# Kernel optimization log

Measured on AMD Instinct MI355X. Metric: run time of the kernel, lower is better.

Reference implementation:

```python
import jax, jax.numpy as jnp
import numpy as np

D = 1024
SCALE = 10.0  # forward does qk.div(1/10) == qk * 10


def setup_inputs() -> dict:
    key = jax.random.key(0)
    ks = jax.random.split(key, 9)
    B, S = 8, 2048
    lim = 1.0 / np.sqrt(D)  # torch Linear default init range
    return {
        "query": jax.random.normal(ks[0], (B, S, D), jnp.float32),
        "key": jax.random.normal(ks[1], (B, S, D), jnp.float32),
        "value": jax.random.normal(ks[2], (B, S, D), jnp.float32),
        "Wq": jax.random.uniform(ks[3], (D, D), jnp.float32, -lim, lim),
        "bq": jax.random.uniform(ks[4], (D,), jnp.float32, -lim, lim),
        "Wk": jax.random.uniform(ks[5], (D, D), jnp.float32, -lim, lim),
        "bk": jax.random.uniform(ks[6], (D,), jnp.float32, -lim, lim),
        "Wv": jax.random.uniform(ks[7], (D, D), jnp.float32, -lim, lim),
        "bv": jax.random.uniform(ks[8], (D,), jnp.float32, -lim, lim),
    }


def reference(query, key, value, Wq, bq, Wk, bk, Wv, bv):
    # torch Linear: x @ W.T + b
    q = jnp.einsum("bsd,ed->bse", query, Wq) + bq
    k = jnp.einsum("bsd,ed->bse", key, Wk) + bk
    v = jnp.einsum("bsd,ed->bse", value, Wv) + bv
    qk = jnp.einsum("bqd,bkd->bqk", q, k)
    scaled_qk = qk * SCALE  # qk.div(1.0 / scale_factor)
    softmax_qk = jax.nn.softmax(scaled_qk, axis=-1)
    # dropout in eval mode == identity (deterministic reference)
    output = jnp.einsum("bqk,bkd->bqd", softmax_qk, v)
    return (output, softmax_qk)
```

## Files before the change

### kernel.cpp

```cpp
#include <hip/hip_runtime.h>

typedef unsigned short u16;
typedef unsigned int u32;
typedef __bf16 bf16x8 __attribute__((ext_vector_type(8)));
typedef float f32x4 __attribute__((ext_vector_type(4)));

__device__ __forceinline__ u16 bf16_rne(float f) {
  u32 u = __float_as_uint(f);
  u += 0x7fffu + ((u >> 16) & 1u);
  return (u16)(u >> 16);
}
__device__ __forceinline__ float bf16_to_f(u16 h) {
  return __uint_as_float(((u32)h) << 16);
}
__device__ __forceinline__ void gload16(const u16* g, u16* l) {
  __builtin_amdgcn_global_load_lds(
      (const __attribute__((address_space(1))) void*)g,
      (__attribute__((address_space(3))) void*)l, 16, 0, 0);
}

__global__ __launch_bounds__(256) void split_kernel(const float* __restrict__ x,
                                                    u16* __restrict__ hi,
                                                    u16* __restrict__ lo, int n8) {
  int i = blockIdx.x * 256 + threadIdx.x;
  if (i >= n8) return;
  float4 a = ((const float4*)x)[2 * i];
  float4 b = ((const float4*)x)[2 * i + 1];
  float v[8] = {a.x, a.y, a.z, a.w, b.x, b.y, b.z, b.w};
  union { u16 u[8]; uint4 q; } H, L;
#pragma unroll
  for (int j = 0; j < 8; ++j) H.u[j] = bf16_rne(v[j]);
  ((uint4*)hi)[i] = H.q;
  if (lo != nullptr) {
#pragma unroll
    for (int j = 0; j < 8; ++j) L.u[j] = bf16_rne(v[j] - bf16_to_f(H.u[j]));
    ((uint4*)lo)[i] = L.q;
  }
}

__global__ __launch_bounds__(256) void transpose_split(const float* __restrict__ in,
                                                       u16* __restrict__ hiT,
                                                       u16* __restrict__ loT) {
  __shared__ float tile[32][33];
  const int t = threadIdx.x;
  const int r0 = blockIdx.y * 32, c0 = blockIdx.x * 32;
  const int x = t & 31, y = t >> 5;
#pragma unroll
  for (int i = 0; i < 4; ++i)
    tile[y + i * 8][x] = in[(size_t)(r0 + y + i * 8) * 1024 + c0 + x];
  __syncthreads();
#pragma unroll
  for (int i = 0; i < 4; ++i) {
    float v = tile[x][y + i * 8];
    u16 h = bf16_rne(v);
    u16 l = bf16_rne(v - bf16_to_f(h));
    size_t o = (size_t)(c0 + y + i * 8) * 1024 + r0 + x;
    hiT[o] = h;
    loT[o] = l;
  }
}

__global__ __launch_bounds__(256) void zero_vec(float* __restrict__ h) {
  h[blockIdx.x * 256 + threadIdx.x] = 0.f;
}

__global__ __launch_bounds__(256) void colvec_kernel(const float* __restrict__ W,
                                                     const float* __restrict__ b,
                                                     float* __restrict__ h) {
  __shared__ float sb[16];
  const int t = threadIdx.x;
  const int e0 = blockIdx.x * 16;
  if (t < 16) sb[t] = b[e0 + t];
  __syncthreads();
  float a0 = 0.f, a1 = 0.f, a2 = 0.f, a3 = 0.f;
#pragma unroll
  for (int i = 0; i < 16; ++i) {
    const float* row = W + (size_t)(e0 + i) * 1024;
    const float be = sb[i];
    a0 += row[t] * be;
    a1 += row[t + 256] * be;
    a2 += row[t + 512] * be;
    a3 += row[t + 768] * be;
  }
  atomicAdd(&h[t], a0);
  atomicAdd(&h[t + 256], a1);
  atomicAdd(&h[t + 512], a2);
  atomicAdd(&h[t + 768], a3);
}

__global__ __launch_bounds__(256) void rowdot_kernel(const float* __restrict__ X,
                                                     const float* __restrict__ h,
                                                     float* __restrict__ w) {
  const int t = threadIdx.x, lane = t & 63, wv = t >> 6;
  const size_t row = (size_t)blockIdx.x * 4 + wv;
  const float4* xr = (const float4*)(X + row * 1024);
  const float4* hr = (const float4*)h;
  float acc = 0.f;
#pragma unroll
  for (int j = 0; j < 4; ++j) {
    float4 a = xr[lane + j * 64];
    float4 b = hr[lane + j * 64];
    acc += a.x * b.x + a.y * b.y + a.z * b.z + a.w * b.w;
  }
#pragma unroll
  for (int o = 32; o > 0; o >>= 1) acc += __shfl_xor(acc, o, 64);
  if (lane == 0) w[row] = acc;
}

template <int NPROD, int EPI>
__global__ __launch_bounds__(256) void gemm_bt(
    const u16* __restrict__ Ah, const u16* __restrict__ Al,
    const u16* __restrict__ Bh, const u16* __restrict__ Bl,
    const float* __restrict__ bias,
    u16* __restrict__ Ch, u16* __restrict__ Cl,
    float* __restrict__ Cf, float scale, int K,
    int lda, int ldb, int ldc,
    long long batchA, long long batchB, long long batchC) {
  __shared__ u16 sAh[4096];
  __shared__ u16 sBh[4096];
  __shared__ u16 sAl[NPROD == 3 ? 4096 : 64];
  __shared__ u16 sBl[NPROD == 3 ? 4096 : 64];

  const int t = threadIdx.x;
  const int w = t >> 6;
  const int lane = t & 63;
  const int m0 = blockIdx.y * 128;
  const int n0 = blockIdx.x * 128;
  const long long z = blockIdx.z;

  Ah += z * batchA;
  Bh += z * batchB;

  const int rS = t >> 2;
  const int cS = (((t & 3) ^ ((t >> 3) & 3))) * 8;
  const u16* pAh = Ah + (size_t)(m0 + rS) * lda + cS;
  const u16* pBh = Bh + (size_t)(n0 + rS) * ldb + cS;
  const u16* pAl = nullptr;
  const u16* pBl = nullptr;
  if constexpr (NPROD == 3) {
    pAl = Al + z * batchA + (size_t)(m0 + rS) * lda + cS;
    pBl = Bl + z * batchB + (size_t)(n0 + rS) * ldb + cS;
  }

  const int wr = (w >> 1) * 64;
  const int wc = (w & 1) * 64;
  const int fr = lane & 15;
  const int cc = lane >> 4;
  const int fk = (cc ^ ((fr >> 1) & 3)) * 8;

  f32x4 acc[4][4];
#pragma unroll
  for (int i = 0; i < 4; ++i)
#pragma unroll
    for (int j = 0; j < 4; ++j) acc[i][j] = (f32x4){0.f, 0.f, 0.f, 0.f};

  for (int k0 = 0; k0 < K; k0 += 32) {
    __syncthreads();
#pragma unroll
    for (int j = 0; j < 2; ++j) {
      gload16(pAh + (size_t)j * 64 * lda + k0, &sAh[j * 2048 + w * 512]);
      gload16(pBh + (size_t)j * 64 * ldb + k0, &sBh[j * 2048 + w * 512]);
      if constexpr (NPROD == 3) {
        gload16(pAl + (size_t)j * 64 * lda + k0, &sAl[j * 2048 + w * 512]);
        gload16(pBl + (size_t)j * 64 * ldb + k0, &sBl[j * 2048 + w * 512]);
      }
    }
    __syncthreads();
    bf16x8 ah[4], bh[4], al[4], bl[4];
#pragma unroll
    for (int i = 0; i < 4; ++i) {
      ah[i] = *(const bf16x8*)&sAh[(wr + i * 16 + fr) * 32 + fk];
      bh[i] = *(const bf16x8*)&sBh[(wc + i * 16 + fr) * 32 + fk];
      if constexpr (NPROD == 3) {
        al[i] = *(const bf16x8*)&sAl[(wr + i * 16 + fr) * 32 + fk];
        bl[i] = *(const bf16x8*)&sBl[(wc + i * 16 + fr) * 32 + fk];
      }
    }
#pragma unroll
    for (int i = 0; i < 4; ++i)
#pragma unroll
      for (int j = 0; j < 4; ++j) {
        acc[i][j] = __builtin_amdgcn_mfma_f32_16x16x32_bf16(ah[i], bh[j], acc[i][j], 0, 0, 0);
        if constexpr (NPROD == 3) {
          acc[i][j] = __builtin_amdgcn_mfma_f32_16x16x32_bf16(ah[i], bl[j], acc[i][j], 0, 0, 0);
          acc[i][j] = __builtin_amdgcn_mfma_f32_16x16x32_bf16(al[i], bh[j], acc[i][j], 0, 0, 0);
        }
      }
  }

  if constexpr (EPI >= 2) Cf += z * batchC;

#pragma unroll
  for (int i = 0; i < 4; ++i) {
    const int row0 = m0 + wr + i * 16 + ((lane >> 4) << 2);
#pragma unroll
    for (int j = 0; j < 4; ++j) {
      const int col = n0 + wc + j * 16 + (lane & 15);
      if constexpr (EPI == 0) {
        const float b = bias ? bias[col] : 0.0f;
#pragma unroll
        for (int r = 0; r < 4; ++r) {
          float c = acc[i][j][r] + b;
          u16 h = bf16_rne(c);
          u16 l = bf16_rne(c - bf16_to_f(h));
          size_t o = (size_t)(row0 + r) * ldc + col;
          Ch[o] = h;
          Cl[o] = l;
        }
      } else if constexpr (EPI == 1) {
        const float b = bias[col];
        ushort4 pk;
        pk.x = bf16_rne(acc[i][j][0] + b);
        pk.y = bf16_rne(acc[i][j][1] + b);
        pk.z = bf16_rne(acc[i][j][2] + b);
        pk.w = bf16_rne(acc[i][j][3] + b);
        const int bb = row0 >> 11;
        const int s = row0 & 2047;
        *(ushort4*)&Ch[(size_t)bb * 2097152 + (size_t)col * 2048 + s] = pk;
      } else if constexpr (EPI == 2) {
#pragma unroll
        for (int r = 0; r < 4; ++r)
          Cf[(size_t)(row0 + r) * ldc + col] = acc[i][j][r] * scale;
      } else {
        const float wv = bias[(size_t)z * 2048 + col];
#pragma unroll
        for (int r = 0; r < 4; ++r)
          Cf[(size_t)(row0 + r) * ldc + col] = (acc[i][j][r] + wv) * scale;
      }
    }
  }
}

template <int NPROD, int EPI>
__global__ __launch_bounds__(512) void gemm256(
    const u16* __restrict__ Ah, const u16* __restrict__ Al,
    const u16* __restrict__ Bh, const u16* __restrict__ Bl,
    const float* __restrict__ bias,
    u16* __restrict__ Ch, u16* __restrict__ Cl,
    float* __restrict__ Cf, float scale, int K,
    int lda, int ldb, int ldc,
    long long batchA, long long batchB, long long batchC) {
  __shared__ u16 sAh[2][8192];
  __shared__ u16 sBh[2][8192];
  __shared__ u16 sAl[NPROD == 3 ? 16384 : 8];
  __shared__ u16 sBl[NPROD == 3 ? 16384 : 8];

  const int t = threadIdx.x;
  const int w = t >> 6;
  const int lane = t & 63;
  const int m0 = blockIdx.y * 256;
  const int n0 = blockIdx.x * 256;
  const long long z = blockIdx.z;

  const int rS = t >> 2;
  const int cS = ((t & 3) ^ ((rS >> 1) & 3)) * 8;
  const u16* pAh = Ah + z * batchA + (size_t)(m0 + rS) * lda + cS;
  const u16* pBh = Bh + z * batchB + (size_t)(n0 + rS) * ldb + cS;
  const u16* pAl = nullptr;
  const u16* pBl = nullptr;
  if constexpr (NPROD == 3) {
    pAl = Al + z * batchA + (size_t)(m0 + rS) * lda + cS;
    pBl = Bl + z * batchB + (size_t)(n0 + rS) * ldb + cS;
  }

  const int wr = (w >> 2) * 128;
  const int wc = (w & 3) * 64;
  const int fr = lane & 15;
  const int fk = (((lane >> 4) ^ ((fr >> 1) & 3)) * 8);

  f32x4 acc[8][4];
#pragma unroll
  for (int i = 0; i < 8; ++i)
#pragma unroll
    for (int j = 0; j < 4; ++j) acc[i][j] = (f32x4){0.f, 0.f, 0.f, 0.f};

  auto STAGE = [&](int b, int k0) {
    gload16(pAh + k0, &sAh[b][w * 512]);
    gload16(pAh + (size_t)128 * lda + k0, &sAh[b][4096 + w * 512]);
    gload16(pBh + k0, &sBh[b][w * 512]);
    gload16(pBh + (size_t)128 * ldb + k0, &sBh[b][4096 + w * 512]);
    if constexpr (NPROD == 3) {
      gload16(pAl + k0, &sAl[b * 8192 + w * 512]);
      gload16(pAl + (size_t)128 * lda + k0, &sAl[b * 8192 + 4096 + w * 512]);
      gload16(pBl + k0, &sBl[b * 8192 + w * 512]);
      gload16(pBl + (size_t)128 * ldb + k0, &sBl[b * 8192 + 4096 + w * 512]);
    }
  };

  STAGE(0, 0);
  const int nt = K >> 5;
  for (int kt = 0; kt < nt; ++kt) {
    const int cur = kt & 1;
    asm volatile("s_waitcnt lgkmcnt(0)\n\ts_barrier" ::: "memory");
    if (kt + 1 < nt) {
      STAGE(cur ^ 1, (kt + 1) << 5);
      if constexpr (NPROD == 3)
        asm volatile("s_waitcnt vmcnt(8)" ::: "memory");
      else
        asm volatile("s_waitcnt vmcnt(4)" ::: "memory");
    } else {
      asm volatile("s_waitcnt vmcnt(0)" ::: "memory");
    }
    asm volatile("s_barrier" ::: "memory");

    bf16x8 bh[4], bl[4];
#pragma unroll
    for (int n = 0; n < 4; ++n) {
      bh[n] = *(const bf16x8*)&sBh[cur][(wc + n * 16 + fr) * 32 + fk];
      if constexpr (NPROD == 3)
        bl[n] = *(const bf16x8*)&sBl[cur * 8192 + (wc + n * 16 + fr) * 32 + fk];
    }
#pragma unroll
    for (int q = 0; q < 4; ++q) {
      bf16x8 a0h = *(const bf16x8*)&sAh[cur][(wr + (2 * q) * 16 + fr) * 32 + fk];
      bf16x8 a1h = *(const bf16x8*)&sAh[cur][(wr + (2 * q + 1) * 16 + fr) * 32 + fk];
      bf16x8 a0l, a1l;
      if constexpr (NPROD == 3) {
        a0l = *(const bf16x8*)&sAl[cur * 8192 + (wr + (2 * q) * 16 + fr) * 32 + fk];
        a1l = *(const bf16x8*)&sAl[cur * 8192 + (wr + (2 * q + 1) * 16 + fr) * 32 + fk];
      }
      __builtin_amdgcn_s_setprio(1);
#pragma unroll
      for (int n = 0; n < 4; ++n) {
        acc[2 * q][n] = __builtin_amdgcn_mfma_f32_16x16x32_bf16(a0h, bh[n], acc[2 * q][n], 0, 0, 0);
        acc[2 * q + 1][n] = __builtin_amdgcn_mfma_f32_16x16x32_bf16(a1h, bh[n], acc[2 * q + 1][n], 0, 0, 0);
      }
      if constexpr (NPROD == 3) {
#pragma unroll
        for (int n = 0; n < 4; ++n) {
          acc[2 * q][n] = __builtin_amdgcn_mfma_f32_16x16x32_bf16(a0h, bl[n], acc[2 * q][n], 0, 0, 0);
          acc[2 * q + 1][n] = __builtin_amdgcn_mfma_f32_16x16x32_bf16(a1h, bl[n], acc[2 * q + 1][n], 0, 0, 0);
        }
#pragma unroll
        for (int n = 0; n < 4; ++n) {
          acc[2 * q][n] = __builtin_amdgcn_mfma_f32_16x16x32_bf16(a0l, bh[n], acc[2 * q][n], 0, 0, 0);
          acc[2 * q + 1][n] = __builtin_amdgcn_mfma_f32_16x16x32_bf16(a1l, bh[n], acc[2 * q + 1][n], 0, 0, 0);
        }
      }
      __builtin_amdgcn_s_setprio(0);
      if (q < 3) asm volatile("s_barrier");
    }
  }

  if constexpr (EPI >= 2) Cf += z * batchC;

#pragma unroll
  for (int i = 0; i < 8; ++i) {
    const int row0 = m0 + wr + i * 16 + ((lane >> 4) << 2);
#pragma unroll
    for (int j = 0; j < 4; ++j) {
      const int col = n0 + wc + j * 16 + (lane & 15);
      if constexpr (EPI == 0) {
        const float bsv = bias ? bias[col] : 0.0f;
#pragma unroll
        for (int r = 0; r < 4; ++r) {
          float c = acc[i][j][r] + bsv;
          u16 h = bf16_rne(c);
          u16 l = bf16_rne(c - bf16_to_f(h));
          size_t o = (size_t)(row0 + r) * ldc + col;
          Ch[o] = h;
          Cl[o] = l;
        }
      } else if constexpr (EPI == 1) {
        const float bsv = bias[col];
        ushort4 pk;
        pk.x = bf16_rne(acc[i][j][0] + bsv);
        pk.y = bf16_rne(acc[i][j][1] + bsv);
        pk.z = bf16_rne(acc[i][j][2] + bsv);
        pk.w = bf16_rne(acc[i][j][3] + bsv);
        const int bb = row0 >> 11;
        const int s = row0 & 2047;
        *(ushort4*)&Ch[(size_t)bb * 2097152 + (size_t)col * 2048 + s] = pk;
      } else if constexpr (EPI == 2) {
#pragma unroll
        for (int r = 0; r < 4; ++r)
          Cf[(size_t)(row0 + r) * ldc + col] = acc[i][j][r] * scale;
      } else {
        const float wv = bias[(size_t)z * 2048 + col];
#pragma unroll
        for (int r = 0; r < 4; ++r)
          Cf[(size_t)(row0 + r) * ldc + col] = (acc[i][j][r] + wv) * scale;
      }
    }
  }
}

__global__ __launch_bounds__(256) void softmax_kernel(float* __restrict__ L,
                                                      u16* __restrict__ P) {
  const size_t row = blockIdx.x;
  float* r = L + row * 2048;
  u16* p = P + row * 2048;
  const int t = threadIdx.x;
  const int w = t >> 6;
  const int lane = t & 63;

  float4 v0 = ((const float4*)r)[2 * t];
  float4 v1 = ((const float4*)r)[2 * t + 1];
  float e[8] = {v0.x, v0.y, v0.z, v0.w, v1.x, v1.y, v1.z, v1.w};

  float vm = e[0];
#pragma unroll
  for (int j = 1; j < 8; ++j) vm = fmaxf(vm, e[j]);
#pragma unroll
  for (int o = 32; o > 0; o >>= 1) vm = fmaxf(vm, __shfl_xor(vm, o, 64));
  __shared__ float redm[4], reds[4];
  if (lane == 0) redm[w] = vm;
  __syncthreads();
  vm = fmaxf(fmaxf(redm[0], redm[1]), fmaxf(redm[2], redm[3]));

  float s = 0.f;
#pragma unroll
  for (int j = 0; j < 8; ++j) {
    e[j] = __expf(e[j] - vm);
    s += e[j];
  }
#pragma unroll
  for (int o = 32; o > 0; o >>= 1) s += __shfl_xor(s, o, 64);
  if (lane == 0) reds[w] = s;
  __syncthreads();
  s = reds[0] + reds[1] + reds[2] + reds[3];
  const float inv = 1.0f / s;

  float4 o0, o1;
  o0.x = e[0] * inv; o0.y = e[1] * inv; o0.z = e[2] * inv; o0.w = e[3] * inv;
  o1.x = e[4] * inv; o1.y = e[5] * inv; o1.z = e[6] * inv; o1.w = e[7] * inv;
  ((float4*)r)[2 * t] = o0;
  ((float4*)r)[2 * t + 1] = o1;
  union { u16 u[8]; uint4 q; } pk;
  pk.u[0] = bf16_rne(o0.x); pk.u[1] = bf16_rne(o0.y);
  pk.u[2] = bf16_rne(o0.z); pk.u[3] = bf16_rne(o0.w);
  pk.u[4] = bf16_rne(o1.x); pk.u[5] = bf16_rne(o1.y);
  pk.u[6] = bf16_rne(o1.z); pk.u[7] = bf16_rne(o1.w);
  ((uint4*)p)[t] = pk.q;
}

extern "C" void kernel_launch(void* const* d_in, const int* in_sizes, int n_in,
                              void* d_out, int out_size, void* d_ws, size_t ws_size,
                              hipStream_t stream) {
  const float* Xq = (const float*)d_in[0];
  const float* Xk = (const float*)d_in[1];
  const float* Xv = (const float*)d_in[2];
  const float* Wq = (const float*)d_in[3];
  const float* bq = (const float*)d_in[4];
  const float* Wk = (const float*)d_in[5];
  const float* bk = (const float*)d_in[6];
  const float* Wv = (const float*)d_in[7];
  const float* bv = (const float*)d_in[8];
  (void)bk;

  char* out = (char*)d_out;
  char* ws = (char*)d_ws;

  u16* T_hi = (u16*)(out + 0);
  u16* T_lo = (u16*)(out + 33554432);
  u16* Xq_hi = (u16*)(out + 67108864);
  u16* Xq_lo = (u16*)(out + 100663296);
  u16* Xv_hi = (u16*)(out + 134217728);
  u16* Mt_hi = (u16*)(out + 167772160);
  u16* Mt_lo = (u16*)(out + 171966464);
  float* logits = (float*)(out + 67108864);
  float* outO = (float*)(out + 0);

  u16* WqT_hi = (u16*)(ws + 0);
  u16* WqT_lo = (u16*)(ws + 2097152);
  u16* WkT_hi = (u16*)(ws + 4194304);
  u16* WkT_lo = (u16*)(ws + 6291456);
  u16* Wv_hi = (u16*)(ws + 8388608);
  u16* P = (u16*)(ws + 0);
  float* hvec = (float*)(ws + 67108864);
  float* wvec = (float*)(ws + 67112960);
  u16* Xk_hi = (u16*)(ws + 67178496);
  u16* Xk_lo = (u16*)(ws + 100732928);
  u16* Vt = (u16*)(ws + 134287360);

  transpose_split<<<dim3(32, 32), 256, 0, stream>>>(Wq, WqT_hi, WqT_lo);
  transpose_split<<<dim3(32, 32), 256, 0, stream>>>(Wk, WkT_hi, WkT_lo);
  zero_vec<<<4, 256, 0, stream>>>(hvec);
  colvec_kernel<<<64, 256, 0, stream>>>(Wk, bq, hvec);
  split_kernel<<<512, 256, 0, stream>>>(Wv, Wv_hi, nullptr, 131072);

  split_kernel<<<8192, 256, 0, stream>>>(Xk, Xk_hi, Xk_lo, 2097152);
  rowdot_kernel<<<4096, 256, 0, stream>>>(Xk, hvec, wvec);
  split_kernel<<<8192, 256, 0, stream>>>(Xq, Xq_hi, Xq_lo, 2097152);
  split_kernel<<<8192, 256, 0, stream>>>(Xv, Xv_hi, nullptr, 2097152);

  gemm_bt<3, 0><<<dim3(8, 8, 1), 256, 0, stream>>>(
      WkT_hi, WkT_lo, WqT_hi, WqT_lo, nullptr, Mt_hi, Mt_lo, nullptr, 1.f,
      1024, 1024, 1024, 1024, 0, 0, 0);
  gemm256<1, 1><<<dim3(4, 64, 1), 512, 0, stream>>>(
      Xv_hi, nullptr, Wv_hi, nullptr, bv, Vt, nullptr, nullptr, 1.f,
      1024, 1024, 1024, 1024, 0, 0, 0);
  gemm256<3, 0><<<dim3(4, 64, 1), 512, 0, stream>>>(
      Xq_hi, Xq_lo, Mt_hi, Mt_lo, nullptr, T_hi, T_lo, nullptr, 1.f,
      1024, 1024, 1024, 1024, 0, 0, 0);
  gemm256<3, 3><<<dim3(8, 8, 8), 512, 0, stream>>>(
      T_hi, T_lo, Xk_hi, Xk_lo, wvec, nullptr, nullptr, logits, 10.f,
      1024, 1024, 1024, 2048, 2048LL * 1024, 2048LL * 1024, 2048LL * 2048);
  softmax_kernel<<<16384, 256, 0, stream>>>(logits, P);
  gemm256<1, 2><<<dim3(4, 8, 8), 512, 0, stream>>>(
      P, nullptr, Vt, nullptr, nullptr, nullptr, nullptr, outO, 1.f,
      2048, 2048, 2048, 1024, 2048LL * 2048, 1024LL * 2048, 2048LL * 1024);
}
```

Before: 970.7 us.

## Interleave next-tile global-to-LDS prefetch with MFMA phases in GEMM main loop

Restructures the double-buffered GEMM K-loop so the next tile's global-to-LDS loads are issued in pieces inside the compute phases (hi parts in the first phase, lo parts in the second) rather than all at once at the top of the iteration. Each phase now loads its LDS fragments, issues its prefetch, syncs with a barrier, then runs MFMAs, using sched_barrier to stop the compiler from reordering. The vmcnt wait moves to the end of the iteration. The single-product path is regrouped into two phases of four A fragments each. The goal is to overlap memory latency with MFMA work and spread out load issue, at the cost of more barriers per iteration.

```diff
diff --git a/kernel.cpp b/kernel.cpp
--- a/kernel.cpp
+++ b/kernel.cpp
@@ -274,58 +274,68 @@
 #pragma unroll
     for (int j = 0; j < 4; ++j) acc[i][j] = (f32x4){0.f, 0.f, 0.f, 0.f};
 
-  auto STAGE = [&](int b, int k0) {
+  auto SAH = [&](int b, int k0) {
     gload16(pAh + k0, &sAh[b][w * 512]);
     gload16(pAh + (size_t)128 * lda + k0, &sAh[b][4096 + w * 512]);
+  };
+  auto SBH = [&](int b, int k0) {
     gload16(pBh + k0, &sBh[b][w * 512]);
     gload16(pBh + (size_t)128 * ldb + k0, &sBh[b][4096 + w * 512]);
-    if constexpr (NPROD == 3) {
-      gload16(pAl + k0, &sAl[b * 8192 + w * 512]);
-      gload16(pAl + (size_t)128 * lda + k0, &sAl[b * 8192 + 4096 + w * 512]);
-      gload16(pBl + k0, &sBl[b * 8192 + w * 512]);
-      gload16(pBl + (size_t)128 * ldb + k0, &sBl[b * 8192 + 4096 + w * 512]);
-    }
   };
-
-  STAGE(0, 0);
+  auto SAL = [&](int b, int k0) {
+    gload16(pAl + k0, &sAl[b * 8192 + w * 512]);
+    gload16(pAl + (size_t)128 * lda + k0, &sAl[b * 8192 + 4096 + w * 512]);
+  };
+  auto SBL = [&](int b, int k0) {
+    gload16(pBl + k0, &sBl[b * 8192 + w * 512]);
+    gload16(pBl + (size_t)128 * ldb + k0, &sBl[b * 8192 + 4096 + w * 512]);
+  };
+
+  SAH(0, 0);
+  SBH(0, 0);
+  if constexpr (NPROD == 3) {
+    SAL(0, 0);
+    SBL(0, 0);
+  }
+  asm volatile("s_waitcnt vmcnt(0)" ::: "memory");
+  __builtin_amdgcn_s_barrier();
+
   const int nt = K >> 5;
   for (int kt = 0; kt < nt; ++kt) {
     const int cur = kt & 1;
-    asm volatile("s_waitcnt lgkmcnt(0)\n\ts_barrier" ::: "memory");
-    if (kt + 1 < nt) {
-      STAGE(cur ^ 1, (kt + 1) << 5);
-      if constexpr (NPROD == 3)
-        asm volatile("s_waitcnt vmcnt(8)" ::: "memory");
-      else
-        asm volatile("s_waitcnt vmcnt(4)" ::: "memory");
-    } else {
-      asm volatile("s_waitcnt vmcnt(0)" ::: "memory");
-    }
-    asm volatile("s_barrier" ::: "memory");
-
-    bf16x8 bh[4], bl[4];
-#pragma unroll
-    for (int n = 0; n < 4; ++n) {
-      bh[n] = *(const bf16x8*)&sBh[cur][(wc + n * 16 + fr) * 32 + fk];
-      if constexpr (NPROD == 3)
-        bl[n] = *(const bf16x8*)&sBl[cur * 8192 + (wc + n * 16 + fr) * 32 + fk];
-    }
-#pragma unroll
-    for (int q = 0; q < 4; ++q) {
-      bf16x8 a0h = *(const bf16x8*)&sAh[cur][(wr + (2 * q) * 16 + fr) * 32 + fk];
-      bf16x8 a1h = *(const bf16x8*)&sAh[cur][(wr + (2 * q + 1) * 16 + fr) * 32 + fk];
-      bf16x8 a0l, a1l;
-      if constexpr (NPROD == 3) {
-        a0l = *(const bf16x8*)&sAl[cur * 8192 + (wr + (2 * q) * 16 + fr) * 32 + fk];
-        a1l = *(const bf16x8*)&sAl[cur * 8192 + (wr + (2 * q + 1) * 16 + fr) * 32 + fk];
-      }
-      __builtin_amdgcn_s_setprio(1);
-#pragma unroll
-      for (int n = 0; n < 4; ++n) {
-        acc[2 * q][n] = __builtin_amdgcn_mfma_f32_16x16x32_bf16(a0h, bh[n], acc[2 * q][n], 0, 0, 0);
-        acc[2 * q + 1][n] = __builtin_amdgcn_mfma_f32_16x16x32_bf16(a1h, bh[n], acc[2 * q + 1][n], 0, 0, 0);
-      }
-      if constexpr (NPROD == 3) {
+    const int nxt = cur ^ 1;
+    const bool pf = (kt + 1) < nt;
+    const int kn = (kt + 1) << 5;
+
+    if constexpr (NPROD == 3) {
+      bf16x8 bh[4], bl[4];
+#pragma unroll
+      for (int q = 0; q < 4; ++q) {
+        if (q == 0) {
+#pragma unroll
+          for (int n = 0; n < 4; ++n) {
+            bh[n] = *(const bf16x8*)&sBh[cur][(wc + n * 16 + fr) * 32 + fk];
+            bl[n] = *(const bf16x8*)&sBl[cur * 8192 + (wc + n * 16 + fr) * 32 + fk];
+          }
+        }
+        bf16x8 a0h = *(const bf16x8*)&sAh[cur][(wr + (2 * q) * 16 + fr) * 32 + fk];
+        bf16x8 a1h = *(const bf16x8*)&sAh[cur][(wr + (2 * q + 1) * 16 + fr) * 32 + fk];
+        bf16x8 a0l = *(const bf16x8*)&sAl[cur * 8192 + (wr + (2 * q) * 16 + fr) * 32 + fk];
+        bf16x8 a1l = *(const bf16x8*)&sAl[cur * 8192 + (wr + (2 * q + 1) * 16 + fr) * 32 + fk];
+        if (pf) {
+          if (q == 0) { SAH(nxt, kn); SBH(nxt, kn); }
+          if (q == 1) { SAL(nxt, kn); SBL(nxt, kn); }
+        }
+        __builtin_amdgcn_sched_barrier(0);
+        __builtin_amdgcn_s_barrier();
+        asm volatile("s_waitcnt lgkmcnt(0)" ::: "memory");
+        __builtin_amdgcn_sched_barrier(0);
+        __builtin_amdgcn_s_setprio(1);
+#pragma unroll
+        for (int n = 0; n < 4; ++n) {
+          acc[2 * q][n] = __builtin_amdgcn_mfma_f32_16x16x32_bf16(a0h, bh[n], acc[2 * q][n], 0, 0, 0);
+          acc[2 * q + 1][n] = __builtin_amdgcn_mfma_f32_16x16x32_bf16(a1h, bh[n], acc[2 * q + 1][n], 0, 0, 0);
+        }
 #pragma unroll
         for (int n = 0; n < 4; ++n) {
           acc[2 * q][n] = __builtin_amdgcn_mfma_f32_16x16x32_bf16(a0h, bl[n], acc[2 * q][n], 0, 0, 0);
@@ -336,9 +346,49 @@
           acc[2 * q][n] = __builtin_amdgcn_mfma_f32_16x16x32_bf16(a0l, bh[n], acc[2 * q][n], 0, 0, 0);
           acc[2 * q + 1][n] = __builtin_amdgcn_mfma_f32_16x16x32_bf16(a1l, bh[n], acc[2 * q + 1][n], 0, 0, 0);
         }
-      }
-      __builtin_amdgcn_s_setprio(0);
-      if (q < 3) asm volatile("s_barrier");
+        __builtin_amdgcn_s_setprio(0);
+        __builtin_amdgcn_sched_barrier(0);
+        if (q == 3) {
+          asm volatile("s_waitcnt vmcnt(0)" ::: "memory");
+          __builtin_amdgcn_sched_barrier(0);
+        }
+        __builtin_amdgcn_s_barrier();
+      }
+    } else {
+      bf16x8 bh[4];
+#pragma unroll
+      for (int q = 0; q < 2; ++q) {
+        if (q == 0) {
+#pragma unroll
+          for (int n = 0; n < 4; ++n)
+            bh[n] = *(const bf16x8*)&sBh[cur][(wc + n * 16 + fr) * 32 + fk];
+        }
+        bf16x8 af[4];
+#pragma unroll
+        for (int i = 0; i < 4; ++i)
+          af[i] = *(const bf16x8*)&sAh[cur][(wr + (4 * q + i) * 16 + fr) * 32 + fk];
+        if (pf) {
+          if (q == 0) SAH(nxt, kn);
+          if (q == 1) SBH(nxt, kn);
+        }
+        __builtin_amdgcn_sched_barrier(0);
+        __builtin_amdgcn_s_barrier();
+        asm volatile("s_waitcnt lgkmcnt(0)" ::: "memory");
+        __builtin_amdgcn_sched_barrier(0);
+        __builtin_amdgcn_s_setprio(1);
+#pragma unroll
+        for (int i = 0; i < 4; ++i)
+#pragma unroll
+          for (int n = 0; n < 4; ++n)
+            acc[4 * q + i][n] = __builtin_amdgcn_mfma_f32_16x16x32_bf16(af[i], bh[n], acc[4 * q + i][n], 0, 0, 0);
+        __builtin_amdgcn_s_setprio(0);
+        __builtin_amdgcn_sched_barrier(0);
+        if (q == 1) {
+          asm volatile("s_waitcnt vmcnt(0)" ::: "memory");
+          __builtin_amdgcn_sched_barrier(0);
+        }
+        __builtin_amdgcn_s_barrier();
+      }
     }
   }
 
```

After: 909.4 us. -6.3%, faster.

## Replace 256x256 GEMM tiles with 128x128 tiles and XCD-aware block remap

Applied to the files above, without the earlier changes.

Replaces the 512-thread 256x256-tile GEMM with a 256-thread 128x128-tile version that uses half the LDS per buffer, and restructures the main loop: the prefetch is issued before the wait, with sched_barriers, and a single trailing barrier replaces the per-subtile barriers. It also remaps linear block IDs so consecutive blocks spread across the 8 XCDs in chunks, for better L2 locality. The aim is higher occupancy and more blocks to fill the CUs. The cost is lower arithmetic intensity per tile and more global and L2 traffic.

```diff
diff --git a/kernel.cpp b/kernel.cpp
--- a/kernel.cpp
+++ b/kernel.cpp
@@ -232,7 +232,7 @@
 }
 
 template <int NPROD, int EPI>
-__global__ __launch_bounds__(512) void gemm256(
+__global__ __launch_bounds__(256) void gemm128(
     const u16* __restrict__ Ah, const u16* __restrict__ Al,
     const u16* __restrict__ Bh, const u16* __restrict__ Bl,
     const float* __restrict__ bias,
@@ -240,20 +240,30 @@
     float* __restrict__ Cf, float scale, int K,
     int lda, int ldb, int ldc,
     long long batchA, long long batchB, long long batchC) {
-  __shared__ u16 sAh[2][8192];
-  __shared__ u16 sBh[2][8192];
-  __shared__ u16 sAl[NPROD == 3 ? 16384 : 8];
-  __shared__ u16 sBl[NPROD == 3 ? 16384 : 8];
+  __shared__ u16 sAh[8192];
+  __shared__ u16 sBh[8192];
+  __shared__ u16 sAl[NPROD == 3 ? 8192 : 8];
+  __shared__ u16 sBl[NPROD == 3 ? 8192 : 8];
 
   const int t = threadIdx.x;
   const int w = t >> 6;
   const int lane = t & 63;
-  const int m0 = blockIdx.y * 256;
-  const int n0 = blockIdx.x * 256;
-  const long long z = blockIdx.z;
+
+  const u32 gx = gridDim.x;
+  const u32 gxy = gridDim.x * gridDim.y;
+  const u32 total = gxy * gridDim.z;
+  const u32 h = blockIdx.x + gridDim.x * (blockIdx.y + gridDim.y * blockIdx.z);
+  const u32 l = (h & 7) * (total >> 3) + (h >> 3);
+  const u32 bz = l / gxy;
+  const u32 rem = l - bz * gxy;
+  const u32 by = rem / gx;
+  const u32 bx = rem - by * gx;
+  const int m0 = by * 128;
+  const int n0 = bx * 128;
+  const long long z = bz;
 
   const int rS = t >> 2;
-  const int cS = ((t & 3) ^ ((rS >> 1) & 3)) * 8;
+  const int cS = (((t & 3) ^ ((t >> 3) & 3))) * 8;
   const u16* pAh = Ah + z * batchA + (size_t)(m0 + rS) * lda + cS;
   const u16* pBh = Bh + z * batchB + (size_t)(n0 + rS) * ldb + cS;
   const u16* pAl = nullptr;
@@ -263,37 +273,41 @@
     pBl = Bl + z * batchB + (size_t)(n0 + rS) * ldb + cS;
   }
 
-  const int wr = (w >> 2) * 128;
-  const int wc = (w & 3) * 64;
+  const int wr = (w >> 1) * 64;
+  const int wc = (w & 1) * 64;
   const int fr = lane & 15;
-  const int fk = (((lane >> 4) ^ ((fr >> 1) & 3)) * 8);
-
-  f32x4 acc[8][4];
-#pragma unroll
-  for (int i = 0; i < 8; ++i)
+  const int cc = lane >> 4;
+  const int fk = (cc ^ ((fr >> 1) & 3)) * 8;
+
+  f32x4 acc[4][4];
+#pragma unroll
+  for (int i = 0; i < 4; ++i)
 #pragma unroll
     for (int j = 0; j < 4; ++j) acc[i][j] = (f32x4){0.f, 0.f, 0.f, 0.f};
 
-  auto STAGE = [&](int b, int k0) {
-    gload16(pAh + k0, &sAh[b][w * 512]);
-    gload16(pAh + (size_t)128 * lda + k0, &sAh[b][4096 + w * 512]);
-    gload16(pBh + k0, &sBh[b][w * 512]);
-    gload16(pBh + (size_t)128 * ldb + k0, &sBh[b][4096 + w * 512]);
-    if constexpr (NPROD == 3) {
-      gload16(pAl + k0, &sAl[b * 8192 + w * 512]);
-      gload16(pAl + (size_t)128 * lda + k0, &sAl[b * 8192 + 4096 + w * 512]);
-      gload16(pBl + k0, &sBl[b * 8192 + w * 512]);
-      gload16(pBl + (size_t)128 * ldb + k0, &sBl[b * 8192 + 4096 + w * 512]);
+  auto STAGE = [&](int bo, int k0) {
+#pragma unroll
+    for (int j = 0; j < 2; ++j) {
+      gload16(pAh + (size_t)j * 64 * lda + k0, &sAh[bo + j * 2048 + w * 512]);
+      gload16(pBh + (size_t)j * 64 * ldb + k0, &sBh[bo + j * 2048 + w * 512]);
+      if constexpr (NPROD == 3) {
+        gload16(pAl + (size_t)j * 64 * lda + k0, &sAl[bo + j * 2048 + w * 512]);
+        gload16(pBl + (size_t)j * 64 * ldb + k0, &sBl[bo + j * 2048 + w * 512]);
+      }
     }
   };
 
   STAGE(0, 0);
+
   const int nt = K >> 5;
   for (int kt = 0; kt < nt; ++kt) {
-    const int cur = kt & 1;
-    asm volatile("s_waitcnt lgkmcnt(0)\n\ts_barrier" ::: "memory");
-    if (kt + 1 < nt) {
-      STAGE(cur ^ 1, (kt + 1) << 5);
+    const int bc = (kt & 1) * 4096;
+    const int bn = 4096 - bc;
+    const bool pf = (kt + 1) < nt;
+
+    if (pf) STAGE(bn, (kt + 1) << 5);
+    __builtin_amdgcn_sched_barrier(0);
+    if (pf) {
       if constexpr (NPROD == 3)
         asm volatile("s_waitcnt vmcnt(8)" ::: "memory");
       else
@@ -301,51 +315,40 @@
     } else {
       asm volatile("s_waitcnt vmcnt(0)" ::: "memory");
     }
+    __builtin_amdgcn_sched_barrier(0);
     asm volatile("s_barrier" ::: "memory");
 
-    bf16x8 bh[4], bl[4];
-#pragma unroll
-    for (int n = 0; n < 4; ++n) {
-      bh[n] = *(const bf16x8*)&sBh[cur][(wc + n * 16 + fr) * 32 + fk];
-      if constexpr (NPROD == 3)
-        bl[n] = *(const bf16x8*)&sBl[cur * 8192 + (wc + n * 16 + fr) * 32 + fk];
-    }
-#pragma unroll
-    for (int q = 0; q < 4; ++q) {
-      bf16x8 a0h = *(const bf16x8*)&sAh[cur][(wr + (2 * q) * 16 + fr) * 32 + fk];
-      bf16x8 a1h = *(const bf16x8*)&sAh[cur][(wr + (2 * q + 1) * 16 + fr) * 32 + fk];
-      bf16x8 a0l, a1l;
+    bf16x8 ah[4], bh[4], al[4], bl[4];
+#pragma unroll
+    for (int i = 0; i < 4; ++i) {
+      ah[i] = *(const bf16x8*)&sAh[bc + (wr + i * 16 + fr) * 32 + fk];
+      bh[i] = *(const bf16x8*)&sBh[bc + (wc + i * 16 + fr) * 32 + fk];
       if constexpr (NPROD == 3) {
-        a0l = *(const bf16x8*)&sAl[cur * 8192 + (wr + (2 * q) * 16 + fr) * 32 + fk];
-        a1l = *(const bf16x8*)&sAl[cur * 8192 + (wr + (2 * q + 1) * 16 + fr) * 32 + fk];
-      }
-      __builtin_amdgcn_s_setprio(1);
-#pragma unroll
-      for (int n = 0; n < 4; ++n) {
-        acc[2 * q][n] = __builtin_amdgcn_mfma_f32_16x16x32_bf16(a0h, bh[n], acc[2 * q][n], 0, 0, 0);
-        acc[2 * q + 1][n] = __builtin_amdgcn_mfma_f32_16x16x32_bf16(a1h, bh[n], acc[2 * q + 1][n], 0, 0, 0);
-      }
-      if constexpr (NPROD == 3) {
-#pragma unroll
-        for (int n = 0; n < 4; ++n) {
-          acc[2 * q][n] = __builtin_amdgcn_mfma_f32_16x16x32_bf16(a0h, bl[n], acc[2 * q][n], 0, 0, 0);
-          acc[2 * q + 1][n] = __builtin_amdgcn_mfma_f32_16x16x32_bf16(a1h, bl[n], acc[2 * q + 1][n], 0, 0, 0);
+        al[i] = *(const bf16x8*)&sAl[bc + (wr + i * 16 + fr) * 32 + fk];
+        bl[i] = *(const bf16x8*)&sBl[bc + (wc + i * 16 + fr) * 32 + fk];
+      }
+    }
+    __builtin_amdgcn_s_setprio(1);
+#pragma unroll
+    for (int i = 0; i < 4; ++i)
+#pragma unroll
+      for (int j = 0; j < 4; ++j) {
+        acc[i][j] = __builtin_amdgcn_mfma_f32_16x16x32_bf16(ah[i], bh[j], acc[i][j], 0, 0, 0);
+        if constexpr (NPROD == 3) {
+          acc[i][j] = __builtin_amdgcn_mfma_f32_16x16x32_bf16(ah[i], bl[j], acc[i][j], 0, 0, 0);
+          acc[i][j] = __builtin_amdgcn_mfma_f32_16x16x32_bf16(al[i], bh[j], acc[i][j], 0, 0, 0);
         }
-#pragma unroll
-        for (int n = 0; n < 4; ++n) {
-          acc[2 * q][n] = __builtin_amdgcn_mfma_f32_16x16x32_bf16(a0l, bh[n], acc[2 * q][n], 0, 0, 0);
-          acc[2 * q + 1][n] = __builtin_amdgcn_mfma_f32_16x16x32_bf16(a1l, bh[n], acc[2 * q + 1][n], 0, 0, 0);
-        }
-      }
-      __builtin_amdgcn_s_setprio(0);
-      if (q < 3) asm volatile("s_barrier");
-    }
+      }
+    __builtin_amdgcn_s_setprio(0);
+    __builtin_amdgcn_sched_barrier(0);
+    asm volatile("s_waitcnt lgkmcnt(0)" ::: "memory");
+    asm volatile("s_barrier" ::: "memory");
   }
 
   if constexpr (EPI >= 2) Cf += z * batchC;
 
 #pragma unroll
-  for (int i = 0; i < 8; ++i) {
+  for (int i = 0; i < 4; ++i) {
     const int row0 = m0 + wr + i * 16 + ((lane >> 4) << 2);
 #pragma unroll
     for (int j = 0; j < 4; ++j) {
@@ -355,11 +358,11 @@
 #pragma unroll
         for (int r = 0; r < 4; ++r) {
           float c = acc[i][j][r] + bsv;
-          u16 h = bf16_rne(c);
-          u16 l = bf16_rne(c - bf16_to_f(h));
+          u16 hh = bf16_rne(c);
+          u16 ll = bf16_rne(c - bf16_to_f(hh));
           size_t o = (size_t)(row0 + r) * ldc + col;
-          Ch[o] = h;
-          Cl[o] = l;
+          Ch[o] = hh;
+          Cl[o] = ll;
         }
       } else if constexpr (EPI == 1) {
         const float bsv = bias[col];
@@ -487,17 +490,17 @@
   gemm_bt<3, 0><<<dim3(8, 8, 1), 256, 0, stream>>>(
       WkT_hi, WkT_lo, WqT_hi, WqT_lo, nullptr, Mt_hi, Mt_lo, nullptr, 1.f,
       1024, 1024, 1024, 1024, 0, 0, 0);
-  gemm256<1, 1><<<dim3(4, 64, 1), 512, 0, stream>>>(
+  gemm128<1, 1><<<dim3(8, 128, 1), 256, 0, stream>>>(
       Xv_hi, nullptr, Wv_hi, nullptr, bv, Vt, nullptr, nullptr, 1.f,
       1024, 1024, 1024, 1024, 0, 0, 0);
-  gemm256<3, 0><<<dim3(4, 64, 1), 512, 0, stream>>>(
+  gemm128<3, 0><<<dim3(8, 128, 1), 256, 0, stream>>>(
       Xq_hi, Xq_lo, Mt_hi, Mt_lo, nullptr, T_hi, T_lo, nullptr, 1.f,
       1024, 1024, 1024, 1024, 0, 0, 0);
-  gemm256<3, 3><<<dim3(8, 8, 8), 512, 0, stream>>>(
+  gemm128<3, 3><<<dim3(16, 16, 8), 256, 0, stream>>>(
       T_hi, T_lo, Xk_hi, Xk_lo, wvec, nullptr, nullptr, logits, 10.f,
       1024, 1024, 1024, 2048, 2048LL * 1024, 2048LL * 1024, 2048LL * 2048);
   softmax_kernel<<<16384, 256, 0, stream>>>(logits, P);
-  gemm256<1, 2><<<dim3(4, 8, 8), 512, 0, stream>>>(
+  gemm128<1, 2><<<dim3(8, 16, 8), 256, 0, stream>>>(
       P, nullptr, Vt, nullptr, nullptr, nullptr, nullptr, outO, 1.f,
       2048, 2048, 2048, 1024, 2048LL * 2048, 1024LL * 2048, 2048LL * 1024);
 }
```

Result: no change. 954.2 us (-1.7%).
